# Kernel optimization log

Hardware: AMD Instinct MI355X
Metric: run time of the kernel (lower is better)

Reference implementation:

```python
import jax, jax.numpy as jnp
import numpy as np

V, D, DFF, E, K, L = 32000, 1024, 4096, 8, 2, 2
B, S = 2, 1024


def _layer_norm(x, scale, bias, eps=1e-5):
    mu = jnp.mean(x, axis=-1, keepdims=True)
    var = jnp.var(x, axis=-1, keepdims=True)
    return (x - mu) * jax.lax.rsqrt(var + eps) * scale + bias


def setup_inputs() -> dict:
    key = jax.random.key(0)
    ks = jax.random.split(key, 16)
    s = 0.02
    return {
        "input_ids": jax.random.randint(ks[0], (B, S), 0, V, dtype=jnp.int32),
        "emb": jax.random.normal(ks[1], (V, D), jnp.float32) * s,
        "t_ln_scale": jnp.ones((L, D), jnp.float32),
        "t_ln_bias": jnp.zeros((L, D), jnp.float32),
        "t_w1": jax.random.normal(ks[2], (L, D, DFF), jnp.float32) * s,
        "t_b1": jnp.zeros((L, DFF), jnp.float32),
        "t_w2": jax.random.normal(ks[3], (L, DFF, D), jnp.float32) * s,
        "t_b2": jnp.zeros((L, D), jnp.float32),
        "Wr": jax.random.normal(ks[4], (D, E), jnp.float32) * s,
        "br": jnp.zeros((E,), jnp.float32),
        "e_w1": jax.random.normal(ks[5], (E, D, DFF), jnp.float32) * s,
        "e_b1": jnp.zeros((E, DFF), jnp.float32),
        "e_w2": jax.random.normal(ks[6], (E, DFF, D), jnp.float32) * s,
        "e_b2": jnp.zeros((E, D), jnp.float32),
        "Wl": jax.random.normal(ks[7], (D, V), jnp.float32) * s,
        "bl": jnp.zeros((V,), jnp.float32),
    }


def reference(input_ids, emb, t_ln_scale, t_ln_bias, t_w1, t_b1, t_w2, t_b2,
              Wr, br, e_w1, e_b1, e_w2, e_b2, Wl, bl):
    # token embeddings: [B,S,D]
    x = emb[input_ids]

    # temporal abstraction: L pre-LN residual MLP blocks
    for l in range(L):
        h = _layer_norm(x, t_ln_scale[l], t_ln_bias[l])
        h = jax.nn.gelu(jnp.einsum('bsd,df->bsf', h, t_w1[l]) + t_b1[l])
        x = x + jnp.einsum('bsf,fd->bsd', h, t_w2[l]) + t_b2[l]

    # router: top-k renormalized softmax over experts, scattered to [B,S,E]
    r_logits = jnp.einsum('bsd,de->bse', x, Wr) + br
    top_vals, top_idx = jax.lax.top_k(r_logits, K)
    top_w = jax.nn.softmax(top_vals, axis=-1)
    routing_weights = jnp.put_along_axis(
        jnp.zeros_like(r_logits), top_idx, top_w, axis=-1, inplace=False)

    # dense all-experts stack: [B,S,E,D]
    h = jax.nn.gelu(jnp.einsum('bsd,edf->bsef', x, e_w1) + e_b1)
    expert_out = jnp.einsum('bsef,efd->bsed', h, e_w2) + e_b2

    # sparse-weighted combine
    y = jnp.einsum('bse,bsed->bsd', routing_weights, expert_out)

    logits = jnp.einsum('bsd,dv->bsv', y, Wl) + bl
    return logits, routing_weights
```

## Files before the change

### kernel.cpp

```cpp
#include <hip/hip_runtime.h>
#include <stdint.h>

typedef __bf16 bf16;
typedef __bf16 bf16x8 __attribute__((ext_vector_type(8)));
typedef float f32x4 __attribute__((ext_vector_type(4)));

#define DEV __device__ __forceinline__

static constexpr int Dm   = 1024;
static constexpr int DFFm = 4096;
static constexpr int Tm   = 2048;
static constexpr int Vm   = 32000;

#define GLOAD_LDS16(g, l)                                                      \
  __builtin_amdgcn_global_load_lds(                                            \
      (const __attribute__((address_space(1))) unsigned int*)(g),              \
      (__attribute__((address_space(3))) unsigned int*)(l), 16, 0, 0)

DEV float gelu_fast(float v) {
  float u = 0.7978845608028654f * (v + 0.044715f * v * v * v);
  float e = __expf(2.0f * u);
  float t = 1.0f - 2.0f / (e + 1.0f);
  return 0.5f * v * (1.0f + t);
}
DEV float gelu_precise(float v) {
  float u = 0.7978845608028654f * (v + 0.044715f * v * v * v);
  return 0.5f * v * (1.0f + tanhf(u));
}

enum { EPI_GELU_SPLIT = 0, EPI_RESID = 1, EPI_GELU_BF16 = 2, EPI_MOE = 3, EPI_BIAS = 4 };

struct GemmP {
  const bf16* Ah; const bf16* Al;
  const bf16* Bh; const bf16* Bl;
  const float* bias;
  const float* resid;
  const float* rwp;
  const int* cnt;
  const int* idx;
  float* outF;
  bf16* outH;
  bf16* outL;
  int K; int N;
  long aBS, bBS, outBS;
  int biasBS;
  int ebase;
};

template <int EPI, bool SPLIT, bool GATHER, bool SWZ>
__launch_bounds__(256, 2)
__global__ void gemm_bt(GemmP p) {
  constexpr bool SPARSE = GATHER || (EPI == EPI_MOE);
  constexpr int LDSN = SPLIT ? 4 : 2;
  __shared__ bf16 lds[LDSN * 4096];
  bf16* ldsAh = lds;
  bf16* ldsBh = lds + 4096;
  bf16* ldsAl = SPLIT ? lds + 8192 : lds;
  bf16* ldsBl = SPLIT ? lds + 12288 : lds;

  const int tid  = threadIdx.x;
  const int lane = tid & 63;
  const int wid  = tid >> 6;
  const int wr   = wid >> 1;
  const int wc   = wid & 1;
  const int z    = blockIdx.z;
  const long K   = p.K;

  int bx = blockIdx.x, by = blockIdx.y;
  if constexpr (SWZ) {
    const int gx = gridDim.x, gy = gridDim.y;
    const int nwg = gx * gy;
    const int id = bx * gy + by;
    const int q = nwg >> 3, r = nwg & 7;
    const int xcd = id & 7, loc = id >> 3;
    const int nid = (xcd < r ? xcd * (q + 1) : r * (q + 1) + (xcd - r) * q) + loc;
    bx = nid / gy; by = nid % gy;
  }

  const long am0 = (long)by * 128;
  const long bn0 = (long)bx * 128;

  int cntE = 0;
  const int* il = nullptr;
  if constexpr (SPARSE) {
    cntE = p.cnt[p.ebase + z];
    if (am0 >= cntE) return;
    il = p.idx + (long)(p.ebase + z) * 2048;
  }

  const int c0 = wid * 64 + lane;
  const int c1 = 256 + wid * 64 + lane;
  const bf16 *aS0, *aS1, *bS0, *bS1;
  const bf16 *aL0 = nullptr, *aL1 = nullptr, *bL0 = nullptr, *bL1 = nullptr;
  {
    const bf16* Bb = p.Bh + (long)z * p.bBS + bn0 * K;
    bS0 = Bb + (long)(c0 >> 2) * K + (c0 & 3) * 8;
    bS1 = Bb + (long)(c1 >> 2) * K + (c1 & 3) * 8;
    if constexpr (GATHER) {
      const int g0 = (int)am0 + (c0 >> 2);
      const int g1 = (int)am0 + (c1 >> 2);
      const long r0 = il[g0 < cntE ? g0 : 0];
      const long r1 = il[g1 < cntE ? g1 : 0];
      aS0 = p.Ah + r0 * K + (c0 & 3) * 8;
      aS1 = p.Ah + r1 * K + (c1 & 3) * 8;
    } else {
      const bf16* Ab = p.Ah + (long)z * p.aBS + am0 * K;
      aS0 = Ab + (long)(c0 >> 2) * K + (c0 & 3) * 8;
      aS1 = Ab + (long)(c1 >> 2) * K + (c1 & 3) * 8;
    }
    if constexpr (SPLIT) {
      const bf16* Abl = p.Al + (long)z * p.aBS + am0 * K;
      const bf16* Bbl = p.Bl + (long)z * p.bBS + bn0 * K;
      aL0 = Abl + (long)(c0 >> 2) * K + (c0 & 3) * 8;
      aL1 = Abl + (long)(c1 >> 2) * K + (c1 & 3) * 8;
      bL0 = Bbl + (long)(c0 >> 2) * K + (c0 & 3) * 8;
      bL1 = Bbl + (long)(c1 >> 2) * K + (c1 & 3) * 8;
    }
  }
  char* dst0 = (char*)(void*)lds + (wid * 64) * 16;
  char* dst1 = (char*)(void*)lds + (256 + wid * 64) * 16;

  f32x4 acc[4][4] = {};

  const int aoff = (wr * 64 + (lane & 15)) * 32 + (lane >> 4) * 8;
  const int boff = (wc * 64 + (lane & 15)) * 32 + (lane >> 4) * 8;

  for (long k0 = 0; k0 < K; k0 += 32) {
    __syncthreads();
    GLOAD_LDS16(aS0 + k0, dst0);
    GLOAD_LDS16(aS1 + k0, dst1);
    GLOAD_LDS16(bS0 + k0, dst0 + 8192);
    GLOAD_LDS16(bS1 + k0, dst1 + 8192);
    if constexpr (SPLIT) {
      GLOAD_LDS16(aL0 + k0, dst0 + 16384);
      GLOAD_LDS16(aL1 + k0, dst1 + 16384);
      GLOAD_LDS16(bL0 + k0, dst0 + 24576);
      GLOAD_LDS16(bL1 + k0, dst1 + 24576);
    }
    __syncthreads();

    bf16x8 ah[4], bh[4];
#pragma unroll
    for (int m = 0; m < 4; ++m) ah[m] = *(const bf16x8*)(ldsAh + aoff + m * 512);
#pragma unroll
    for (int n = 0; n < 4; ++n) bh[n] = *(const bf16x8*)(ldsBh + boff + n * 512);
    if constexpr (SPLIT) {
      bf16x8 al[4], bl[4];
#pragma unroll
      for (int m = 0; m < 4; ++m) al[m] = *(const bf16x8*)(ldsAl + aoff + m * 512);
#pragma unroll
      for (int n = 0; n < 4; ++n) bl[n] = *(const bf16x8*)(ldsBl + boff + n * 512);
#pragma unroll
      for (int m = 0; m < 4; ++m)
#pragma unroll
        for (int n = 0; n < 4; ++n) {
          acc[m][n] = __builtin_amdgcn_mfma_f32_16x16x32_bf16(ah[m], bh[n], acc[m][n], 0, 0, 0);
          acc[m][n] = __builtin_amdgcn_mfma_f32_16x16x32_bf16(ah[m], bl[n], acc[m][n], 0, 0, 0);
          acc[m][n] = __builtin_amdgcn_mfma_f32_16x16x32_bf16(al[m], bh[n], acc[m][n], 0, 0, 0);
        }
    } else {
#pragma unroll
      for (int m = 0; m < 4; ++m)
#pragma unroll
        for (int n = 0; n < 4; ++n)
          acc[m][n] = __builtin_amdgcn_mfma_f32_16x16x32_bf16(ah[m], bh[n], acc[m][n], 0, 0, 0);
    }
  }

  const float* bias = p.bias + (long)z * p.biasBS;
  const long N = p.N;

#pragma unroll
  for (int m = 0; m < 4; ++m) {
#pragma unroll
    for (int n = 0; n < 4; ++n) {
      const long col = bn0 + wc * 64 + n * 16 + (lane & 15);
      const float bv = bias[col];
#pragma unroll
      for (int r = 0; r < 4; ++r) {
        const long row = am0 + wr * 64 + m * 16 + (lane >> 4) * 4 + r;
        float v = acc[m][n][r] + bv;
        if constexpr (EPI == EPI_GELU_SPLIT) {
          float g = gelu_precise(v);
          bf16 h = (bf16)g;
          long o = row * N + col;
          p.outH[o] = h;
          p.outL[o] = (bf16)(g - (float)h);
        } else if constexpr (EPI == EPI_RESID) {
          long o = row * N + col;
          p.outF[o] = p.resid[o] + v;
        } else if constexpr (EPI == EPI_GELU_BF16) {
          long o = (long)z * p.outBS + row * N + col;
          p.outH[o] = (bf16)gelu_fast(v);
        } else if constexpr (EPI == EPI_MOE) {
          if (row < cntE) {
            const int tok = il[row];
            const float wgt = p.rwp[(long)tok * 8 + p.ebase + z];
            atomicAdd(p.outF + (long)tok * N + col, wgt * v);
          }
        } else {
          p.outF[row * N + col] = v;
        }
      }
    }
  }
}

template <bool SPLITOUT>
__global__ void transpose_cvt(const float* __restrict__ in, bf16* __restrict__ outh,
                              bf16* __restrict__ outl, int R, int C, long inBS, long outBS) {
  __shared__ float tile[32][33];
  const float* inp = in + (long)blockIdx.z * inBS;
  const long c0 = (long)blockIdx.x * 32;
  const long r0 = (long)blockIdx.y * 32;
  const int tx = threadIdx.x;
  const int ty = threadIdx.y;
#pragma unroll
  for (int i = 0; i < 4; ++i) {
    int r = ty + i * 8;
    tile[r][tx] = inp[(r0 + r) * (long)C + c0 + tx];
  }
  __syncthreads();
  const long ob = (long)blockIdx.z * outBS;
#pragma unroll
  for (int i = 0; i < 4; ++i) {
    int c = ty + i * 8;
    float v = tile[tx][c];
    bf16 h = (bf16)v;
    long o = ob + (c0 + c) * (long)R + r0 + tx;
    outh[o] = h;
    if constexpr (SPLITOUT) outl[o] = (bf16)(v - (float)h);
  }
}

__global__ void embed_kernel(const int* __restrict__ ids, const float* __restrict__ emb,
                             float* __restrict__ x) {
  const long t = blockIdx.x;
  const int id = ids[t];
  ((float4*)(x + t * 1024))[threadIdx.x] = ((const float4*)(emb + (long)id * 1024))[threadIdx.x];
}

__global__ void ln_split_kernel(const float* __restrict__ x, const float* __restrict__ sc,
                                const float* __restrict__ bi, bf16* __restrict__ oh,
                                bf16* __restrict__ ol) {
  const long t = blockIdx.x;
  const int tid = threadIdx.x;
  const int lane = tid & 63, wid = tid >> 6;
  float4 a = ((const float4*)(x + t * 1024))[tid];
  float s = a.x + a.y + a.z + a.w;
  float q = a.x * a.x + a.y * a.y + a.z * a.z + a.w * a.w;
#pragma unroll
  for (int off = 32; off; off >>= 1) {
    s += __shfl_down(s, off);
    q += __shfl_down(q, off);
  }
  __shared__ float sr[4], qr[4];
  if (lane == 0) { sr[wid] = s; qr[wid] = q; }
  __syncthreads();
  s = sr[0] + sr[1] + sr[2] + sr[3];
  q = qr[0] + qr[1] + qr[2] + qr[3];
  const float mu = s * (1.0f / 1024.0f);
  const float var = q * (1.0f / 1024.0f) - mu * mu;
  const float rs = rsqrtf(var + 1e-5f);
#pragma unroll
  for (int j = 0; j < 4; ++j) {
    const int d = tid * 4 + j;
    const float g = (((const float*)&a)[j] - mu) * rs * sc[d] + bi[d];
    const bf16 h = (bf16)g;
    oh[t * 1024 + d] = h;
    ol[t * 1024 + d] = (bf16)(g - (float)h);
  }
}

__global__ void router_kernel(const float* __restrict__ x, const float* __restrict__ Wr,
                              const float* __restrict__ br, float* __restrict__ rwo,
                              int* __restrict__ top2) {
  const long t = blockIdx.x;
  const int lane = threadIdx.x;
  float acc[8];
#pragma unroll
  for (int e = 0; e < 8; ++e) acc[e] = 0.0f;
  const float4* xr = (const float4*)(x + t * 1024);
#pragma unroll
  for (int j = 0; j < 4; ++j) {
    const int d4 = j * 64 + lane;
    float4 xv = xr[d4];
#pragma unroll
    for (int u = 0; u < 4; ++u) {
      const float xs = ((const float*)&xv)[u];
      const float4* wp = (const float4*)(Wr + (long)(d4 * 4 + u) * 8);
      float4 w0 = wp[0], w1 = wp[1];
      acc[0] += xs * w0.x; acc[1] += xs * w0.y; acc[2] += xs * w0.z; acc[3] += xs * w0.w;
      acc[4] += xs * w1.x; acc[5] += xs * w1.y; acc[6] += xs * w1.z; acc[7] += xs * w1.w;
    }
  }
#pragma unroll
  for (int off = 32; off; off >>= 1)
#pragma unroll
    for (int e = 0; e < 8; ++e) acc[e] += __shfl_down(acc[e], off);
  if (lane == 0) {
    float v[8];
#pragma unroll
    for (int e = 0; e < 8; ++e) v[e] = acc[e] + br[e];
    int i0 = 0; float v0 = v[0];
    for (int e = 1; e < 8; ++e) if (v[e] > v0) { v0 = v[e]; i0 = e; }
    int i1 = -1; float v1 = -3.4e38f;
    for (int e = 0; e < 8; ++e) if (e != i0 && v[e] > v1) { v1 = v[e]; i1 = e; }
    float e1 = expf(v1 - v0);
    float den = 1.0f + e1;
    float w0 = 1.0f / den, w1 = e1 / den;
    float* o = rwo + t * 8;
#pragma unroll
    for (int e = 0; e < 8; ++e) o[e] = (e == i0) ? w0 : (e == i1 ? w1 : 0.0f);
    top2[t] = i0 | (i1 << 8);
  }
}

__global__ void build_lists(const int* __restrict__ top2, int* __restrict__ cnt,
                            int* __restrict__ idx) {
  const int t = blockIdx.x * 256 + threadIdx.x;
  const int rec = top2[t];
  const int e0 = rec & 255, e1 = (rec >> 8) & 255;
  int p0 = atomicAdd(&cnt[e0], 1);
  idx[e0 * 2048 + p0] = t;
  int p1 = atomicAdd(&cnt[e1], 1);
  idx[e1 * 2048 + p1] = t;
}

__global__ void cvt_bf16_kernel(const float* __restrict__ in, bf16* __restrict__ out, long n) {
  long i = ((long)blockIdx.x * blockDim.x + threadIdx.x) * 8;
  if (i >= n) return;
  float4 a = *(const float4*)(in + i);
  float4 b = *(const float4*)(in + i + 4);
  bf16x8 o;
  o[0] = (bf16)a.x; o[1] = (bf16)a.y; o[2] = (bf16)a.z; o[3] = (bf16)a.w;
  o[4] = (bf16)b.x; o[5] = (bf16)b.y; o[6] = (bf16)b.z; o[7] = (bf16)b.w;
  *(bf16x8*)(out + i) = o;
}

extern "C" void kernel_launch(void* const* d_in, const int* in_sizes, int n_in,
                              void* d_out, int out_size, void* d_ws, size_t ws_size,
                              hipStream_t stream) {
  (void)in_sizes; (void)n_in; (void)out_size; (void)ws_size;
  const int*   ids  = (const int*)d_in[0];
  const float* emb  = (const float*)d_in[1];
  const float* tlns = (const float*)d_in[2];
  const float* tlnb = (const float*)d_in[3];
  const float* tw1  = (const float*)d_in[4];
  const float* tb1  = (const float*)d_in[5];
  const float* tw2  = (const float*)d_in[6];
  const float* tb2  = (const float*)d_in[7];
  const float* Wr   = (const float*)d_in[8];
  const float* br   = (const float*)d_in[9];
  const float* ew1  = (const float*)d_in[10];
  const float* eb1  = (const float*)d_in[11];
  const float* ew2  = (const float*)d_in[12];
  const float* eb2  = (const float*)d_in[13];
  const float* Wl   = (const float*)d_in[14];
  const float* bl   = (const float*)d_in[15];

  float* logits = (float*)d_out;
  float* rwout  = (float*)d_out + (long)Tm * Vm;

  size_t off = 0;
  auto take = [&](size_t bytes) {
    void* pp = (char*)d_ws + off;
    off += (bytes + 255) & ~(size_t)255;
    return pp;
  };
  float* X    = (float*)take((size_t)Tm * Dm * 4);
  bf16*  XB   = (bf16*) take((size_t)Tm * Dm * 2);
  float* Y    = (float*)take((size_t)Tm * Dm * 4);
  bf16*  YB   = (bf16*) take((size_t)Tm * Dm * 2);
  bf16*  Breg = (bf16*) take((size_t)4 * DFFm * Dm * 2);
  bf16*  Creg = (bf16*) take((size_t)(2L * Tm * Dm + 2L * Tm * DFFm) * 2);
  bf16*  Dreg = (bf16*) take((size_t)4 * Tm * DFFm * 2);
  int*   top2 = (int*)  take((size_t)Tm * 4);
  int*   cnt  = (int*)  take(8 * 4);
  int*   idxl = (int*)  take((size_t)8 * Tm * 4);

  bf16* TW1h = Breg;
  bf16* TW1l = Breg + (long)DFFm * Dm;
  bf16* TW2h = Breg + 2L * DFFm * Dm;
  bf16* TW2l = Breg + 3L * DFFm * Dm;
  bf16* EW1T = Breg;
  bf16* HLNh = Creg;
  bf16* HLNl = Creg + (long)Tm * Dm;
  bf16* HTh  = Creg + 2L * Tm * Dm;
  bf16* HTl  = HTh + (long)Tm * DFFm;
  bf16* EW2T = Creg;
  bf16* HE   = Dreg;
  bf16* WLT  = Dreg;

  embed_kernel<<<dim3(Tm), dim3(256), 0, stream>>>(ids, emb, X);

  for (int l = 0; l < 2; ++l) {
    transpose_cvt<true><<<dim3(DFFm / 32, Dm / 32, 1), dim3(32, 8), 0, stream>>>(
        tw1 + (long)l * Dm * DFFm, TW1h, TW1l, Dm, DFFm, 0, 0);
    transpose_cvt<true><<<dim3(Dm / 32, DFFm / 32, 1), dim3(32, 8), 0, stream>>>(
        tw2 + (long)l * DFFm * Dm, TW2h, TW2l, DFFm, Dm, 0, 0);
    ln_split_kernel<<<dim3(Tm), dim3(256), 0, stream>>>(X, tlns + l * Dm, tlnb + l * Dm,
                                                        HLNh, HLNl);
    GemmP p1{};
    p1.Ah = HLNh; p1.Al = HLNl; p1.Bh = TW1h; p1.Bl = TW1l;
    p1.bias = tb1 + (long)l * DFFm;
    p1.outH = HTh; p1.outL = HTl;
    p1.K = Dm; p1.N = DFFm;
    gemm_bt<EPI_GELU_SPLIT, true, false, false>
        <<<dim3(DFFm / 128, Tm / 128, 1), dim3(256), 0, stream>>>(p1);

    GemmP p2{};
    p2.Ah = HTh; p2.Al = HTl; p2.Bh = TW2h; p2.Bl = TW2l;
    p2.bias = tb2 + (long)l * Dm;
    p2.resid = X; p2.outF = X;
    p2.K = DFFm; p2.N = Dm;
    gemm_bt<EPI_RESID, true, false, false>
        <<<dim3(Dm / 128, Tm / 128, 1), dim3(256), 0, stream>>>(p2);
  }

  router_kernel<<<dim3(Tm), dim3(64), 0, stream>>>(X, Wr, br, rwout, top2);
  hipMemsetAsync(cnt, 0, 8 * 4, stream);
  build_lists<<<dim3(Tm / 256), dim3(256), 0, stream>>>(top2, cnt, idxl);
  cvt_bf16_kernel<<<dim3(Tm * Dm / (256 * 8)), dim3(256), 0, stream>>>(X, XB, (long)Tm * Dm);
  hipMemsetAsync(Y, 0, (size_t)Tm * Dm * 4, stream);

  for (int q = 0; q < 2; ++q) {
    transpose_cvt<false><<<dim3(DFFm / 32, Dm / 32, 4), dim3(32, 8), 0, stream>>>(
        ew1 + (long)q * 4 * Dm * DFFm, EW1T, nullptr, Dm, DFFm, (long)Dm * DFFm,
        (long)DFFm * Dm);
    transpose_cvt<false><<<dim3(Dm / 32, DFFm / 32, 4), dim3(32, 8), 0, stream>>>(
        ew2 + (long)q * 4 * DFFm * Dm, EW2T, nullptr, DFFm, Dm, (long)DFFm * Dm,
        (long)Dm * DFFm);

    GemmP pe1{};
    pe1.Ah = XB; pe1.Bh = EW1T;
    pe1.bias = eb1 + (long)q * 4 * DFFm; pe1.biasBS = DFFm;
    pe1.outH = HE; pe1.outBS = (long)Tm * DFFm;
    pe1.aBS = 0; pe1.bBS = (long)DFFm * Dm;
    pe1.cnt = cnt; pe1.idx = idxl; pe1.ebase = q * 4;
    pe1.K = Dm; pe1.N = DFFm;
    gemm_bt<EPI_GELU_BF16, false, true, false>
        <<<dim3(DFFm / 128, Tm / 128, 4), dim3(256), 0, stream>>>(pe1);

    GemmP pe2{};
    pe2.Ah = HE; pe2.aBS = (long)Tm * DFFm;
    pe2.Bh = EW2T; pe2.bBS = (long)Dm * DFFm;
    pe2.bias = eb2 + (long)q * 4 * Dm; pe2.biasBS = Dm;
    pe2.rwp = rwout; pe2.cnt = cnt; pe2.idx = idxl; pe2.ebase = q * 4;
    pe2.outF = Y;
    pe2.K = DFFm; pe2.N = Dm;
    gemm_bt<EPI_MOE, false, false, false>
        <<<dim3(Dm / 128, Tm / 128, 4), dim3(256), 0, stream>>>(pe2);
  }

  cvt_bf16_kernel<<<dim3(Tm * Dm / (256 * 8)), dim3(256), 0, stream>>>(Y, YB, (long)Tm * Dm);
  transpose_cvt<false><<<dim3(Vm / 32, Dm / 32, 1), dim3(32, 8), 0, stream>>>(
      Wl, WLT, nullptr, Dm, Vm, 0, 0);
  GemmP pl{};
  pl.Ah = YB; pl.Bh = WLT; pl.bias = bl;
  pl.outF = logits;
  pl.K = Dm; pl.N = Vm;
  gemm_bt<EPI_BIAS, false, false, true>
      <<<dim3(Vm / 128, Tm / 128, 1), dim3(256), 0, stream>>>(pl);
}
```

Baseline: 1.192 ms.

## Replace split-bf16 triple MFMA with augmented-K layout and split-K residual GEMM

Stores the hi/lo bf16 split operands as concatenated K-augmented rows ([h, l, h] against [h, h, l]), so the three-term split product becomes a single plain bf16 GEMM over 3K with half the LDS. The second temporal GEMM is split in two along K across blockIdx.z and accumulates into X with atomics, which raises parallelism for the small 1024-wide output. It also turns on the XCD-aware block swizzle for all GEMMs, changes the swizzle's linear order, and uses nontemporal stores for the logits. In exchange the operands take more memory traffic, the two halves are summed by float atomics in nondeterministic order, and the scratch layout is rebuilt around fixed byte offsets.

```diff
diff --git a/kernel.cpp b/kernel.cpp
--- a/kernel.cpp
+++ b/kernel.cpp
@@ -31,32 +31,28 @@
 enum { EPI_GELU_SPLIT = 0, EPI_RESID = 1, EPI_GELU_BF16 = 2, EPI_MOE = 3, EPI_BIAS = 4 };
 
 struct GemmP {
-  const bf16* Ah; const bf16* Al;
-  const bf16* Bh; const bf16* Bl;
+  const bf16* Ah;
+  const bf16* Bh;
   const float* bias;
-  const float* resid;
   const float* rwp;
   const int* cnt;
   const int* idx;
   float* outF;
   bf16* outH;
-  bf16* outL;
   int K; int N;
+  int lda; int ldb; int ldo;
   long aBS, bBS, outBS;
   int biasBS;
   int ebase;
 };
 
-template <int EPI, bool SPLIT, bool GATHER, bool SWZ>
+template <int EPI, bool GATHER, bool SWZ>
 __launch_bounds__(256, 2)
 __global__ void gemm_bt(GemmP p) {
   constexpr bool SPARSE = GATHER || (EPI == EPI_MOE);
-  constexpr int LDSN = SPLIT ? 4 : 2;
-  __shared__ bf16 lds[LDSN * 4096];
-  bf16* ldsAh = lds;
-  bf16* ldsBh = lds + 4096;
-  bf16* ldsAl = SPLIT ? lds + 8192 : lds;
-  bf16* ldsBl = SPLIT ? lds + 12288 : lds;
+  __shared__ bf16 lds[8192];
+  bf16* ldsA = lds;
+  bf16* ldsB = lds + 4096;
 
   const int tid  = threadIdx.x;
   const int lane = tid & 63;
@@ -64,15 +60,14 @@
   const int wr   = wid >> 1;
   const int wc   = wid & 1;
   const int z    = blockIdx.z;
-  const long K   = p.K;
 
   int bx = blockIdx.x, by = blockIdx.y;
   if constexpr (SWZ) {
     const int gx = gridDim.x, gy = gridDim.y;
     const int nwg = gx * gy;
-    const int id = bx * gy + by;
+    const int lin = by * gx + bx;
     const int q = nwg >> 3, r = nwg & 7;
-    const int xcd = id & 7, loc = id >> 3;
+    const int xcd = lin & 7, loc = lin >> 3;
     const int nid = (xcd < r ? xcd * (q + 1) : r * (q + 1) + (xcd - r) * q) + loc;
     bx = nid / gy; by = nid % gy;
   }
@@ -88,33 +83,27 @@
     il = p.idx + (long)(p.ebase + z) * 2048;
   }
 
+  const long lda = p.lda, ldb = p.ldb;
+  const long K = p.K;
+
   const int c0 = wid * 64 + lane;
   const int c1 = 256 + wid * 64 + lane;
   const bf16 *aS0, *aS1, *bS0, *bS1;
-  const bf16 *aL0 = nullptr, *aL1 = nullptr, *bL0 = nullptr, *bL1 = nullptr;
   {
-    const bf16* Bb = p.Bh + (long)z * p.bBS + bn0 * K;
-    bS0 = Bb + (long)(c0 >> 2) * K + (c0 & 3) * 8;
-    bS1 = Bb + (long)(c1 >> 2) * K + (c1 & 3) * 8;
+    const bf16* Bb = p.Bh + (long)z * p.bBS + bn0 * ldb;
+    bS0 = Bb + (long)(c0 >> 2) * ldb + (c0 & 3) * 8;
+    bS1 = Bb + (long)(c1 >> 2) * ldb + (c1 & 3) * 8;
     if constexpr (GATHER) {
       const int g0 = (int)am0 + (c0 >> 2);
       const int g1 = (int)am0 + (c1 >> 2);
       const long r0 = il[g0 < cntE ? g0 : 0];
       const long r1 = il[g1 < cntE ? g1 : 0];
-      aS0 = p.Ah + r0 * K + (c0 & 3) * 8;
-      aS1 = p.Ah + r1 * K + (c1 & 3) * 8;
+      aS0 = p.Ah + r0 * lda + (c0 & 3) * 8;
+      aS1 = p.Ah + r1 * lda + (c1 & 3) * 8;
     } else {
-      const bf16* Ab = p.Ah + (long)z * p.aBS + am0 * K;
-      aS0 = Ab + (long)(c0 >> 2) * K + (c0 & 3) * 8;
-      aS1 = Ab + (long)(c1 >> 2) * K + (c1 & 3) * 8;
-    }
-    if constexpr (SPLIT) {
-      const bf16* Abl = p.Al + (long)z * p.aBS + am0 * K;
-      const bf16* Bbl = p.Bl + (long)z * p.bBS + bn0 * K;
-      aL0 = Abl + (long)(c0 >> 2) * K + (c0 & 3) * 8;
-      aL1 = Abl + (long)(c1 >> 2) * K + (c1 & 3) * 8;
-      bL0 = Bbl + (long)(c0 >> 2) * K + (c0 & 3) * 8;
-      bL1 = Bbl + (long)(c1 >> 2) * K + (c1 & 3) * 8;
+      const bf16* Ab = p.Ah + (long)z * p.aBS + am0 * lda;
+      aS0 = Ab + (long)(c0 >> 2) * lda + (c0 & 3) * 8;
+      aS1 = Ab + (long)(c1 >> 2) * lda + (c1 & 3) * 8;
     }
   }
   char* dst0 = (char*)(void*)lds + (wid * 64) * 16;
@@ -131,43 +120,20 @@
     GLOAD_LDS16(aS1 + k0, dst1);
     GLOAD_LDS16(bS0 + k0, dst0 + 8192);
     GLOAD_LDS16(bS1 + k0, dst1 + 8192);
-    if constexpr (SPLIT) {
-      GLOAD_LDS16(aL0 + k0, dst0 + 16384);
-      GLOAD_LDS16(aL1 + k0, dst1 + 16384);
-      GLOAD_LDS16(bL0 + k0, dst0 + 24576);
-      GLOAD_LDS16(bL1 + k0, dst1 + 24576);
-    }
     __syncthreads();
 
-    bf16x8 ah[4], bh[4];
-#pragma unroll
-    for (int m = 0; m < 4; ++m) ah[m] = *(const bf16x8*)(ldsAh + aoff + m * 512);
-#pragma unroll
-    for (int n = 0; n < 4; ++n) bh[n] = *(const bf16x8*)(ldsBh + boff + n * 512);
-    if constexpr (SPLIT) {
-      bf16x8 al[4], bl[4];
-#pragma unroll
-      for (int m = 0; m < 4; ++m) al[m] = *(const bf16x8*)(ldsAl + aoff + m * 512);
-#pragma unroll
-      for (int n = 0; n < 4; ++n) bl[n] = *(const bf16x8*)(ldsBl + boff + n * 512);
-#pragma unroll
-      for (int m = 0; m < 4; ++m)
-#pragma unroll
-        for (int n = 0; n < 4; ++n) {
-          acc[m][n] = __builtin_amdgcn_mfma_f32_16x16x32_bf16(ah[m], bh[n], acc[m][n], 0, 0, 0);
-          acc[m][n] = __builtin_amdgcn_mfma_f32_16x16x32_bf16(ah[m], bl[n], acc[m][n], 0, 0, 0);
-          acc[m][n] = __builtin_amdgcn_mfma_f32_16x16x32_bf16(al[m], bh[n], acc[m][n], 0, 0, 0);
-        }
-    } else {
-#pragma unroll
-      for (int m = 0; m < 4; ++m)
-#pragma unroll
-        for (int n = 0; n < 4; ++n)
-          acc[m][n] = __builtin_amdgcn_mfma_f32_16x16x32_bf16(ah[m], bh[n], acc[m][n], 0, 0, 0);
-    }
-  }
-
-  const float* bias = p.bias + (long)z * p.biasBS;
+    bf16x8 a[4], b[4];
+#pragma unroll
+    for (int m = 0; m < 4; ++m) a[m] = *(const bf16x8*)(ldsA + aoff + m * 512);
+#pragma unroll
+    for (int n = 0; n < 4; ++n) b[n] = *(const bf16x8*)(ldsB + boff + n * 512);
+#pragma unroll
+    for (int m = 0; m < 4; ++m)
+#pragma unroll
+      for (int n = 0; n < 4; ++n)
+        acc[m][n] = __builtin_amdgcn_mfma_f32_16x16x32_bf16(a[m], b[n], acc[m][n], 0, 0, 0);
+  }
+
   const long N = p.N;
 
 #pragma unroll
@@ -175,7 +141,9 @@
 #pragma unroll
     for (int n = 0; n < 4; ++n) {
       const long col = bn0 + wc * 64 + n * 16 + (lane & 15);
-      const float bv = bias[col];
+      float bv;
+      if constexpr (EPI == EPI_RESID) bv = (z == 0) ? p.bias[col] : 0.0f;
+      else bv = p.bias[(long)z * p.biasBS + col];
 #pragma unroll
       for (int r = 0; r < 4; ++r) {
         const long row = am0 + wr * 64 + m * 16 + (lane >> 4) * 4 + r;
@@ -183,12 +151,12 @@
         if constexpr (EPI == EPI_GELU_SPLIT) {
           float g = gelu_precise(v);
           bf16 h = (bf16)g;
-          long o = row * N + col;
+          long o = row * (long)p.ldo + col;
           p.outH[o] = h;
-          p.outL[o] = (bf16)(g - (float)h);
+          p.outH[o + N] = (bf16)(g - (float)h);
+          p.outH[o + 2 * N] = h;
         } else if constexpr (EPI == EPI_RESID) {
-          long o = row * N + col;
-          p.outF[o] = p.resid[o] + v;
+          atomicAdd(p.outF + row * N + col, v);
         } else if constexpr (EPI == EPI_GELU_BF16) {
           long o = (long)z * p.outBS + row * N + col;
           p.outH[o] = (bf16)gelu_fast(v);
@@ -199,16 +167,16 @@
             atomicAdd(p.outF + (long)tok * N + col, wgt * v);
           }
         } else {
-          p.outF[row * N + col] = v;
+          __builtin_nontemporal_store(v, p.outF + row * N + col);
         }
       }
     }
   }
 }
 
-template <bool SPLITOUT>
-__global__ void transpose_cvt(const float* __restrict__ in, bf16* __restrict__ outh,
-                              bf16* __restrict__ outl, int R, int C, long inBS, long outBS) {
+template <bool AUG>
+__global__ void transpose_cvt(const float* __restrict__ in, bf16* __restrict__ out,
+                              int R, int C, long inBS, long outBS) {
   __shared__ float tile[32][33];
   const float* inp = in + (long)blockIdx.z * inBS;
   const long c0 = (long)blockIdx.x * 32;
@@ -222,14 +190,18 @@
   }
   __syncthreads();
   const long ob = (long)blockIdx.z * outBS;
+  const long stride = AUG ? 3L * R : (long)R;
 #pragma unroll
   for (int i = 0; i < 4; ++i) {
     int c = ty + i * 8;
     float v = tile[tx][c];
     bf16 h = (bf16)v;
-    long o = ob + (c0 + c) * (long)R + r0 + tx;
-    outh[o] = h;
-    if constexpr (SPLITOUT) outl[o] = (bf16)(v - (float)h);
+    long o = ob + (c0 + c) * stride + r0 + tx;
+    out[o] = h;
+    if constexpr (AUG) {
+      out[o + R] = h;
+      out[o + 2 * R] = (bf16)(v - (float)h);
+    }
   }
 }
 
@@ -240,9 +212,8 @@
   ((float4*)(x + t * 1024))[threadIdx.x] = ((const float4*)(emb + (long)id * 1024))[threadIdx.x];
 }
 
-__global__ void ln_split_kernel(const float* __restrict__ x, const float* __restrict__ sc,
-                                const float* __restrict__ bi, bf16* __restrict__ oh,
-                                bf16* __restrict__ ol) {
+__global__ void ln_aug_kernel(const float* __restrict__ x, const float* __restrict__ sc,
+                              const float* __restrict__ bi, bf16* __restrict__ oa) {
   const long t = blockIdx.x;
   const int tid = threadIdx.x;
   const int lane = tid & 63, wid = tid >> 6;
@@ -267,8 +238,9 @@
     const int d = tid * 4 + j;
     const float g = (((const float*)&a)[j] - mu) * rs * sc[d] + bi[d];
     const bf16 h = (bf16)g;
-    oh[t * 1024 + d] = h;
-    ol[t * 1024 + d] = (bf16)(g - (float)h);
+    oa[t * 3072 + d] = h;
+    oa[t * 3072 + 1024 + d] = (bf16)(g - (float)h);
+    oa[t * 3072 + 2048 + d] = h;
   }
 }
 
@@ -372,50 +344,45 @@
   bf16*  XB   = (bf16*) take((size_t)Tm * Dm * 2);
   float* Y    = (float*)take((size_t)Tm * Dm * 4);
   bf16*  YB   = (bf16*) take((size_t)Tm * Dm * 2);
-  bf16*  Breg = (bf16*) take((size_t)4 * DFFm * Dm * 2);
-  bf16*  Creg = (bf16*) take((size_t)(2L * Tm * Dm + 2L * Tm * DFFm) * 2);
-  bf16*  Dreg = (bf16*) take((size_t)4 * Tm * DFFm * 2);
   int*   top2 = (int*)  take((size_t)Tm * 4);
   int*   cnt  = (int*)  take(8 * 4);
   int*   idxl = (int*)  take((size_t)8 * Tm * 4);
-
-  bf16* TW1h = Breg;
-  bf16* TW1l = Breg + (long)DFFm * Dm;
-  bf16* TW2h = Breg + 2L * DFFm * Dm;
-  bf16* TW2l = Breg + 3L * DFFm * Dm;
-  bf16* EW1T = Breg;
-  bf16* HLNh = Creg;
-  bf16* HLNl = Creg + (long)Tm * Dm;
-  bf16* HTh  = Creg + 2L * Tm * Dm;
-  bf16* HTl  = HTh + (long)Tm * DFFm;
-  bf16* EW2T = Creg;
-  bf16* HE   = Dreg;
-  bf16* WLT  = Dreg;
+  char*  S    = (char*) take(134217728);
+
+  bf16* A1  = (bf16*)S;
+  bf16* W1A = (bf16*)(S + 12582912);
+  bf16* W2A = (bf16*)(S + 12582912 + 25165824);
+  bf16* HTA = (bf16*)(S + 12582912 + 2 * 25165824);
+  bf16* EW1T = (bf16*)S;
+  bf16* HE   = (bf16*)(S + 33554432);
+  bf16* EW2T = (bf16*)(S + 100663296);
+  bf16* WLT  = (bf16*)S;
 
   embed_kernel<<<dim3(Tm), dim3(256), 0, stream>>>(ids, emb, X);
 
   for (int l = 0; l < 2; ++l) {
     transpose_cvt<true><<<dim3(DFFm / 32, Dm / 32, 1), dim3(32, 8), 0, stream>>>(
-        tw1 + (long)l * Dm * DFFm, TW1h, TW1l, Dm, DFFm, 0, 0);
+        tw1 + (long)l * Dm * DFFm, W1A, Dm, DFFm, 0, 0);
     transpose_cvt<true><<<dim3(Dm / 32, DFFm / 32, 1), dim3(32, 8), 0, stream>>>(
-        tw2 + (long)l * DFFm * Dm, TW2h, TW2l, DFFm, Dm, 0, 0);
-    ln_split_kernel<<<dim3(Tm), dim3(256), 0, stream>>>(X, tlns + l * Dm, tlnb + l * Dm,
-                                                        HLNh, HLNl);
+        tw2 + (long)l * DFFm * Dm, W2A, DFFm, Dm, 0, 0);
+    ln_aug_kernel<<<dim3(Tm), dim3(256), 0, stream>>>(X, tlns + l * Dm, tlnb + l * Dm, A1);
+
     GemmP p1{};
-    p1.Ah = HLNh; p1.Al = HLNl; p1.Bh = TW1h; p1.Bl = TW1l;
+    p1.Ah = A1; p1.Bh = W1A;
     p1.bias = tb1 + (long)l * DFFm;
-    p1.outH = HTh; p1.outL = HTl;
-    p1.K = Dm; p1.N = DFFm;
-    gemm_bt<EPI_GELU_SPLIT, true, false, false>
+    p1.outH = HTA;
+    p1.K = 3072; p1.N = DFFm; p1.lda = 3072; p1.ldb = 3072; p1.ldo = 3 * DFFm;
+    gemm_bt<EPI_GELU_SPLIT, false, true>
         <<<dim3(DFFm / 128, Tm / 128, 1), dim3(256), 0, stream>>>(p1);
 
     GemmP p2{};
-    p2.Ah = HTh; p2.Al = HTl; p2.Bh = TW2h; p2.Bl = TW2l;
+    p2.Ah = HTA; p2.Bh = W2A;
     p2.bias = tb2 + (long)l * Dm;
-    p2.resid = X; p2.outF = X;
-    p2.K = DFFm; p2.N = Dm;
-    gemm_bt<EPI_RESID, true, false, false>
-        <<<dim3(Dm / 128, Tm / 128, 1), dim3(256), 0, stream>>>(p2);
+    p2.outF = X;
+    p2.K = 6144; p2.N = Dm; p2.lda = 12288; p2.ldb = 12288;
+    p2.aBS = 6144; p2.bBS = 6144;
+    gemm_bt<EPI_RESID, false, true>
+        <<<dim3(Dm / 128, Tm / 128, 2), dim3(256), 0, stream>>>(p2);
   }
 
   router_kernel<<<dim3(Tm), dim3(64), 0, stream>>>(X, Wr, br, rwout, top2);
@@ -426,11 +393,9 @@
 
   for (int q = 0; q < 2; ++q) {
     transpose_cvt<false><<<dim3(DFFm / 32, Dm / 32, 4), dim3(32, 8), 0, stream>>>(
-        ew1 + (long)q * 4 * Dm * DFFm, EW1T, nullptr, Dm, DFFm, (long)Dm * DFFm,
-        (long)DFFm * Dm);
+        ew1 + (long)q * 4 * Dm * DFFm, EW1T, Dm, DFFm, (long)Dm * DFFm, (long)DFFm * Dm);
     transpose_cvt<false><<<dim3(Dm / 32, DFFm / 32, 4), dim3(32, 8), 0, stream>>>(
-        ew2 + (long)q * 4 * DFFm * Dm, EW2T, nullptr, DFFm, Dm, (long)DFFm * Dm,
-        (long)Dm * DFFm);
+        ew2 + (long)q * 4 * DFFm * Dm, EW2T, DFFm, Dm, (long)DFFm * Dm, (long)Dm * DFFm);
 
     GemmP pe1{};
     pe1.Ah = XB; pe1.Bh = EW1T;
@@ -438,8 +403,8 @@
     pe1.outH = HE; pe1.outBS = (long)Tm * DFFm;
     pe1.aBS = 0; pe1.bBS = (long)DFFm * Dm;
     pe1.cnt = cnt; pe1.idx = idxl; pe1.ebase = q * 4;
-    pe1.K = Dm; pe1.N = DFFm;
-    gemm_bt<EPI_GELU_BF16, false, true, false>
+    pe1.K = Dm; pe1.N = DFFm; pe1.lda = Dm; pe1.ldb = Dm;
+    gemm_bt<EPI_GELU_BF16, true, true>
         <<<dim3(DFFm / 128, Tm / 128, 4), dim3(256), 0, stream>>>(pe1);
 
     GemmP pe2{};
@@ -448,18 +413,18 @@
     pe2.bias = eb2 + (long)q * 4 * Dm; pe2.biasBS = Dm;
     pe2.rwp = rwout; pe2.cnt = cnt; pe2.idx = idxl; pe2.ebase = q * 4;
     pe2.outF = Y;
-    pe2.K = DFFm; pe2.N = Dm;
-    gemm_bt<EPI_MOE, false, false, false>
+    pe2.K = DFFm; pe2.N = Dm; pe2.lda = DFFm; pe2.ldb = DFFm;
+    gemm_bt<EPI_MOE, false, true>
         <<<dim3(Dm / 128, Tm / 128, 4), dim3(256), 0, stream>>>(pe2);
   }
 
   cvt_bf16_kernel<<<dim3(Tm * Dm / (256 * 8)), dim3(256), 0, stream>>>(Y, YB, (long)Tm * Dm);
   transpose_cvt<false><<<dim3(Vm / 32, Dm / 32, 1), dim3(32, 8), 0, stream>>>(
-      Wl, WLT, nullptr, Dm, Vm, 0, 0);
+      Wl, WLT, Dm, Vm, 0, 0);
   GemmP pl{};
   pl.Ah = YB; pl.Bh = WLT; pl.bias = bl;
   pl.outF = logits;
-  pl.K = Dm; pl.N = Vm;
-  gemm_bt<EPI_BIAS, false, false, true>
+  pl.K = Dm; pl.N = Vm; pl.lda = Dm; pl.ldb = Dm;
+  gemm_bt<EPI_BIAS, false, true>
       <<<dim3(Vm / 128, Tm / 128, 1), dim3(256), 0, stream>>>(pl);
 }
```

After: 1.192 ms. Within noise of the previous version (+0.0%).
